# Performance work log

Measured on AMD Instinct MI355X. Metric: run time of the kernel, lower is better.

Reference implementation:

```python
import jax, jax.numpy as jnp
import numpy as np
from bisect import bisect

# hyperparameters (from init_kwargs)
DELTA = 1e-4
GAMMA = 0.1
UTILITY_SCALE = -0.01
PRIORITY_RAIL = 0.5
LOSS_BALANCE = 1.0
ALPHA_ELU = 1.0
ENTROPY_THRESHOLDS = [0, 10, 50]
ENTROPY_LEVELS = [0.0, 0.05, 0.1, 1.0]
MASK_LEVEL = 10000.0

N = 512


def setup_inputs() -> dict:
    key = jax.random.key(0)
    k1, k2, k3, k4 = jax.random.split(key, 4)
    soft_adj = jax.random.uniform(k1, (N, N), dtype=jnp.float32)
    # original adjacency is a binary {0,1} float mask
    original_adj = (jax.random.uniform(k2, (N, N)) > 0.5).astype(jnp.float32)
    distances = jax.random.uniform(k3, (N, N), dtype=jnp.float32) * 100.0
    flow = jax.random.uniform(k4, (N, N), dtype=jnp.float32) * 10.0
    epoch = 20  # python int, selects entropy penalty level via bisect
    return {"soft_adj": soft_adj, "original_adj": original_adj,
            "distances": distances, "flow": flow, "epoch": epoch}


def _shortest_path(soft_adj, distances):
    """Soft (softmin via logsumexp) Floyd-Warshall all-pairs shortest path."""
    W = distances / (soft_adj + DELTA)          # [N, N] effective edge weights
    n = W.shape[0]
    w0 = W * (1.0 - jnp.eye(n, dtype=W.dtype))  # zero diagonal

    def step(w, k):
        # softmin(w, w[:,k,None] + w[None,k,:]) without materializing a stack
        path_through_k = w[:, k][:, None] + w[k, :][None, :]
        w_new = -GAMMA * jnp.logaddexp(-w / GAMMA, -path_through_k / GAMMA)
        return w_new, None

    w_dist, _ = jax.lax.scan(step, w0, jnp.arange(n))
    return w_dist


def reference(soft_adj, original_adj, distances, flow, epoch):
    loss_cost = jnp.sum(soft_adj * distances)

    shortest_paths = _shortest_path(soft_adj, distances)

    exp_ut_rail = jnp.exp(UTILITY_SCALE * shortest_paths * PRIORITY_RAIL)
    exp_ut_base = jnp.exp(UTILITY_SCALE * distances)
    choice_matrix = exp_ut_rail / (exp_ut_rail + exp_ut_base)
    distance_saved = distances - PRIORITY_RAIL * shortest_paths
    utility_gain = flow * choice_matrix * distance_saved
    utility_gain = jax.nn.elu(utility_gain, alpha=ALPHA_ELU) + ALPHA_ELU

    inverse_soft = jnp.eye(soft_adj.shape[0], dtype=soft_adj.dtype) - soft_adj
    entropy_loss = jnp.sum(jnp.square(soft_adj * inverse_soft))
    entropy_scale = ENTROPY_LEVELS[bisect(ENTROPY_THRESHOLDS, epoch)]

    mask_loss = jnp.sum(soft_adj * (1.0 - original_adj))

    return (loss_cost
            + LOSS_BALANCE * jnp.sum(utility_gain)
            + entropy_loss * entropy_scale
            + MASK_LEVEL * mask_loss)
```

## Files before the change

kernel.cpp:

```cpp
#include <hip/hip_runtime.h>
#include <math.h>

#define NN 512
#define KP 64
#define NPANEL 8
#define NTHR 256
#define NBLK 256
#define TRUNITS (448 * 112)

#define D_   0
#define V_   4160
#define B2_  8320
#define UB_  12672
#define SB_  17024
#define H_   21376
#define LDSN 25728

__device__ __forceinline__ float einit(const float* s, const float* dI, int i, int j) {
  float w = dI[i * NN + j] / (s[i * NN + j] + 1e-4f);
  if (i == j) w = 0.f;
  return expf(-10.f * w);
}

template <int M0, int M1>
__device__ __forceinline__ void evolve_seg(float* lds, float (&x)[64], int tid) {
#pragma unroll
  for (int m = M0; m < M1; ++m) {
    const float xm = x[m];
    lds[H_ + m * 68 + tid] = xm;
#pragma unroll
    for (int a = m + 1; a < 64; ++a) {
      const int sa = __builtin_amdgcn_readlane(__float_as_int(x[a]), m);
      x[a] += __int_as_float(sa) * xm;
    }
  }
}

__device__ __forceinline__ void pgemm_chunk(float* lds, int cch, int tt2, int h) {
  const int mb = cch * 16;
  const int r = 32 * h + (tt2 & 31);
  const int g = tt2 >> 5;
  const int m0c = mb + 4 * g;
  const int vb = V_ + r * 65;
  float a0 = lds[vb + m0c + 0], a1 = lds[vb + m0c + 1];
  float a2 = lds[vb + m0c + 2], a3 = lds[vb + m0c + 3];
  for (int mp = 0; mp < mb; ++mp) {
    const float vr = lds[vb + mp];
    const float4 u4 = *(const float4*)&lds[H_ + mp * 68 + m0c];
    a0 += vr * u4.x; a1 += vr * u4.y; a2 += vr * u4.z; a3 += vr * u4.w;
  }
  lds[vb + m0c + 0] = a0; lds[vb + m0c + 1] = a1;
  lds[vb + m0c + 2] = a2; lds[vb + m0c + 3] = a3;
}

__device__ __forceinline__ void micro_chunk(float* lds, int cch, int t3, int h) {
  const int mb = cch * 16;
  const int r = 32 * h + t3;
  const int vb = V_ + r * 65 + mb;
  float v[16];
#pragma unroll
  for (int u2 = 0; u2 < 16; ++u2) v[u2] = lds[vb + u2];
#pragma unroll
  for (int mp = 0; mp < 15; ++mp) {
    const float vmp = v[mp];
#pragma unroll
    for (int m2 = mp + 1; m2 < 16; ++m2)
      v[m2] += vmp * lds[H_ + (mb + mp) * 68 + (mb + m2)];
  }
#pragma unroll
  for (int u2 = 0; u2 < 16; ++u2) lds[vb + u2] = v[u2];
}

__global__ __launch_bounds__(NTHR) void fw_phase(
    const float* __restrict__ s, const float* __restrict__ dI,
    float* __restrict__ E, float* __restrict__ Cs, float* __restrict__ Rs,
    float* __restrict__ out, int p) {
  __shared__ __align__(16) float lds[LDSN];
  const int blk = blockIdx.x, tid = threadIdx.x;
  const int k0 = p * KP;

  if (blk >= 32) {
    const int gt = (blk - 32) * NTHR + tid;
    if (p == 0) {
      if (blk == 32 && tid == 0) out[0] = 0.f;
      if (gt < TRUNITS) {
        const int ii = gt / 112;
        const int jj = gt - ii * 112;
        const int i = ii + KP;
        const int j = (jj + 16) << 2;
        const int idx = i * NN + j;
        const float4 sv = *(const float4*)(s + idx);
        const float4 dv = *(const float4*)(dI + idx);
        float w0 = dv.x / (sv.x + 1e-4f); if (i == j + 0) w0 = 0.f;
        float w1 = dv.y / (sv.y + 1e-4f); if (i == j + 1) w1 = 0.f;
        float w2 = dv.z / (sv.z + 1e-4f); if (i == j + 2) w2 = 0.f;
        float w3 = dv.w / (sv.w + 1e-4f); if (i == j + 3) w3 = 0.f;
        *(float4*)(E + idx) = make_float4(expf(-10.f * w0), expf(-10.f * w1),
                                          expf(-10.f * w2), expf(-10.f * w3));
      }
    } else if (gt < TRUNITS) {
      const int ii = gt / 112;
      const int jj = gt - ii * 112;
      const int i = (ii < k0) ? ii : ii + KP;
      const int j = ((jj < (p << 4)) ? jj : jj + 16) << 2;
      const int idx = i * NN + j;
      const float* Cprev = Cs + (size_t)(p - 1) * (NN * KP);
      const float* Rprev = Rs + (size_t)(p - 1) * (KP * NN);
      float4 acc = *(const float4*)(E + idx);
      const float* crow = Cprev + (size_t)i * KP;
      const float* rcol = Rprev + j;
#pragma unroll 8
      for (int r = 0; r < KP; ++r) {
        const float cv = crow[r];
        const float4 rv = *(const float4*)(rcol + (size_t)r * NN);
        acc.x += cv * rv.x; acc.y += cv * rv.y;
        acc.z += cv * rv.z; acc.w += cv * rv.w;
      }
      *(float4*)(E + idx) = acc;
    }
    return;
  }

  const bool isC = (blk < 16);
  const int sb = (blk >> 1) & 7;
  const int h = blk & 1;
  const int sOff = sb * KP;
  const bool haveSl = (sb != p);
  const float* Cprev = Cs + (size_t)(p - 1) * (NN * KP);
  const float* Rprev = Rs + (size_t)(p - 1) * (KP * NN);

  if (p == 0) {
    for (int e = tid; e < 4096; e += NTHR) {
      const int a = e >> 6, b = e & 63;
      const float v = einit(s, dI, a, b);
      lds[D_ + a * 65 + b] = v;
      if (blk == 0) E[a * NN + b] = v;
    }
    if (haveSl) {
      if (isC) {
        for (int e = tid; e < 2048; e += NTHR) {
          const int a = 32 * h + (e >> 6), b = e & 63;
          const float v = einit(s, dI, sOff + a, b);
          lds[V_ + a * 65 + b] = v;
          E[(sOff + a) * NN + b] = v;
        }
      } else {
        for (int e = tid; e < 2048; e += NTHR) {
          const int m = e >> 5, j = 32 * h + (e & 31);
          const float v = einit(s, dI, m, sOff + j);
          lds[V_ + j * 65 + m] = v;
          E[m * NN + (sOff + j)] = v;
        }
      }
    }
  } else {
#pragma unroll
    for (int k = 0; k < 4; ++k) {
      const int e4 = tid + k * NTHR;
      const int a = e4 >> 4, b4 = (e4 & 15) << 2;
      *(float4*)&lds[B2_ + a * 68 + b4] =
          *(const float4*)(Cprev + (size_t)(k0 + a) * KP + b4);
      *(float4*)&lds[UB_ + a * 68 + b4] =
          *(const float4*)(Rprev + (size_t)a * NN + (k0 + b4));
      if (haveSl) {
        if (isC)
          *(float4*)&lds[SB_ + a * 68 + b4] =
              *(const float4*)(Cprev + (size_t)(sOff + a) * KP + b4);
        else
          *(float4*)&lds[SB_ + a * 68 + b4] =
              *(const float4*)(Rprev + (size_t)a * NN + (sOff + b4));
      }
    }
    __syncthreads();
    {
      const int r0 = (tid >> 4) << 2, m0 = (tid & 15) << 2;
      float acc[4][4];
#pragma unroll
      for (int i2 = 0; i2 < 4; ++i2) {
        const float4 ev = *(const float4*)(E + (size_t)(k0 + r0 + i2) * NN + (k0 + m0));
        acc[i2][0] = ev.x; acc[i2][1] = ev.y; acc[i2][2] = ev.z; acc[i2][3] = ev.w;
      }
      for (int rr = 0; rr < KP; rr += 4) {
        float4 av[4];
#pragma unroll
        for (int i2 = 0; i2 < 4; ++i2)
          av[i2] = *(const float4*)&lds[B2_ + (r0 + i2) * 68 + rr];
#pragma unroll
        for (int k = 0; k < 4; ++k) {
          const float4 b4 = *(const float4*)&lds[UB_ + (rr + k) * 68 + m0];
#pragma unroll
          for (int i2 = 0; i2 < 4; ++i2) {
            const float a = (k == 0) ? av[i2].x : (k == 1) ? av[i2].y
                          : (k == 2) ? av[i2].z : av[i2].w;
            acc[i2][0] += a * b4.x; acc[i2][1] += a * b4.y;
            acc[i2][2] += a * b4.z; acc[i2][3] += a * b4.w;
          }
        }
      }
#pragma unroll
      for (int i2 = 0; i2 < 4; ++i2)
#pragma unroll
        for (int j2 = 0; j2 < 4; ++j2)
          lds[D_ + (r0 + i2) * 65 + (m0 + j2)] = acc[i2][j2];
    }
  }
  __syncthreads();

  float x[64];
  if (tid < 64) {
    if (isC) {
#pragma unroll
      for (int a = 0; a < 64; ++a) x[a] = lds[D_ + a * 65 + tid];
    } else {
#pragma unroll
      for (int a = 0; a < 64; ++a) x[a] = lds[D_ + tid * 65 + a];
    }
    evolve_seg<0, 16>(lds, x, tid);
  } else if (tid < 192) {
    const int tt = tid - 64;
    if (haveSl && p > 0) {
      float acc[4][4];
      if (isC) {
        const int r0 = 32 * h + ((tt >> 4) << 2);
        const int m0 = (tt & 15) << 2;
#pragma unroll
        for (int i2 = 0; i2 < 4; ++i2) {
          const float4 ev = *(const float4*)(E + (size_t)(sOff + r0 + i2) * NN + (k0 + m0));
          acc[i2][0] = ev.x; acc[i2][1] = ev.y; acc[i2][2] = ev.z; acc[i2][3] = ev.w;
        }
        for (int rr = 0; rr < KP; rr += 4) {
          float4 av[4];
#pragma unroll
          for (int i2 = 0; i2 < 4; ++i2)
            av[i2] = *(const float4*)&lds[SB_ + (r0 + i2) * 68 + rr];
#pragma unroll
          for (int k = 0; k < 4; ++k) {
            const float4 b4 = *(const float4*)&lds[UB_ + (rr + k) * 68 + m0];
#pragma unroll
            for (int i2 = 0; i2 < 4; ++i2) {
              const float a = (k == 0) ? av[i2].x : (k == 1) ? av[i2].y
                            : (k == 2) ? av[i2].z : av[i2].w;
              acc[i2][0] += a * b4.x; acc[i2][1] += a * b4.y;
              acc[i2][2] += a * b4.z; acc[i2][3] += a * b4.w;
            }
          }
        }
#pragma unroll
        for (int i2 = 0; i2 < 4; ++i2) {
          *(float4*)(E + (size_t)(sOff + r0 + i2) * NN + (k0 + m0)) =
              make_float4(acc[i2][0], acc[i2][1], acc[i2][2], acc[i2][3]);
#pragma unroll
          for (int j2 = 0; j2 < 4; ++j2)
            lds[V_ + (r0 + i2) * 65 + (m0 + j2)] = acc[i2][j2];
        }
      } else {
        const int r0 = (tt & 15) << 2;
        const int c0 = 32 * h + ((tt >> 4) << 2);
#pragma unroll
        for (int i2 = 0; i2 < 4; ++i2) {
          const float4 ev = *(const float4*)(E + (size_t)(k0 + r0 + i2) * NN + (sOff + c0));
          acc[i2][0] = ev.x; acc[i2][1] = ev.y; acc[i2][2] = ev.z; acc[i2][3] = ev.w;
        }
        for (int rr = 0; rr < KP; rr += 4) {
          float4 av[4];
#pragma unroll
          for (int i2 = 0; i2 < 4; ++i2)
            av[i2] = *(const float4*)&lds[B2_ + (r0 + i2) * 68 + rr];
#pragma unroll
          for (int k = 0; k < 4; ++k) {
            const float4 b4 = *(const float4*)&lds[SB_ + (rr + k) * 68 + c0];
#pragma unroll
            for (int i2 = 0; i2 < 4; ++i2) {
              const float a = (k == 0) ? av[i2].x : (k == 1) ? av[i2].y
                            : (k == 2) ? av[i2].z : av[i2].w;
              acc[i2][0] += a * b4.x; acc[i2][1] += a * b4.y;
              acc[i2][2] += a * b4.z; acc[i2][3] += a * b4.w;
            }
          }
        }
#pragma unroll
        for (int i2 = 0; i2 < 4; ++i2) {
          *(float4*)(E + (size_t)(k0 + r0 + i2) * NN + (sOff + c0)) =
              make_float4(acc[i2][0], acc[i2][1], acc[i2][2], acc[i2][3]);
#pragma unroll
          for (int j2 = 0; j2 < 4; ++j2)
            lds[V_ + (c0 + j2) * 65 + (r0 + i2)] = acc[i2][j2];
        }
      }
    } else if (!haveSl) {
      for (int e = tt; e < 4096; e += 128) {
        const int a = e >> 6, b = e & 63;
        lds[V_ + a * 65 + b] = isC ? lds[D_ + a * 65 + b] : lds[D_ + b * 65 + a];
      }
    }
  }
  __syncthreads();

  if (tid < 64) evolve_seg<16, 32>(lds, x, tid);
  else if (tid >= 192 && tid < 224) micro_chunk(lds, 0, tid - 192, h);
  __syncthreads();

  if (tid < 64) evolve_seg<32, 48>(lds, x, tid);
  else if (tid < 192) pgemm_chunk(lds, 1, tid - 64, h);
  __syncthreads();

  if (tid < 64) evolve_seg<48, 64>(lds, x, tid);
  else if (tid >= 192 && tid < 224) micro_chunk(lds, 1, tid - 192, h);
  __syncthreads();

  if (tid >= 64 && tid < 192) pgemm_chunk(lds, 2, tid - 64, h);
  __syncthreads();
  if (tid >= 192 && tid < 224) micro_chunk(lds, 2, tid - 192, h);
  __syncthreads();
  if (tid >= 64 && tid < 192) pgemm_chunk(lds, 3, tid - 64, h);
  __syncthreads();
  if (tid >= 192 && tid < 224) micro_chunk(lds, 3, tid - 192, h);
  __syncthreads();

  float* Cp = Cs + (size_t)p * (NN * KP);
  float* Rp = Rs + (size_t)p * (KP * NN);
  if (isC) {
    for (int e = tid; e < 2048; e += NTHR) {
      const int a = 32 * h + (e >> 6), b = e & 63;
      Cp[(size_t)(sOff + a) * KP + b] = lds[V_ + a * 65 + b];
    }
  } else {
    for (int e = tid; e < 2048; e += NTHR) {
      const int m = e >> 5, j = 32 * h + (e & 31);
      Rp[(size_t)m * NN + (sOff + j)] = lds[V_ + j * 65 + m];
    }
  }
}

__device__ __forceinline__ float loss_elem(float Ev, float sv, float ov,
                                           float dv, float fv, int i, int j,
                                           float esc) {
  const float sp = (Ev > 0.f) ? (-0.1f * logf(Ev)) : 1e9f;
  const float ur = expf(-0.005f * sp);
  const float ub = expf(-0.01f * dv);
  const float choice = ur / (ur + ub);
  const float ug = fv * choice * (dv - 0.5f * sp);
  const float util = (ug > 0.f) ? (ug + 1.f) : expf(ug);
  const float ent = sv * (((i == j) ? 1.f : 0.f) - sv);
  return sv * dv + util + esc * ent * ent + 10000.f * (sv * (1.f - ov));
}

__global__ __launch_bounds__(NTHR) void k_loss(
    const float* __restrict__ s, const float* __restrict__ o,
    const float* __restrict__ dI, const float* __restrict__ f,
    const int* __restrict__ ep, const float* __restrict__ E,
    const float* __restrict__ Cs, const float* __restrict__ Rs,
    float* __restrict__ out) {
  __shared__ float red[NTHR];
  const int tid = threadIdx.x;
  const int g = blockIdx.x * NTHR + tid;
  const int idx0 = g * 4;
  const int i = idx0 >> 9;
  const int j = idx0 & (NN - 1);
  const float* C7 = Cs + (size_t)7 * (NN * KP);
  const float* R7 = Rs + (size_t)7 * (KP * NN);
  float4 acc = *(const float4*)(E + idx0);
  {
    const float* crow = C7 + (size_t)i * KP;
    const float* rcol = R7 + j;
#pragma unroll 8
    for (int r = 0; r < KP; ++r) {
      const float cv = crow[r];
      const float4 rv = *(const float4*)(rcol + (size_t)r * NN);
      acc.x += cv * rv.x; acc.y += cv * rv.y;
      acc.z += cv * rv.z; acc.w += cv * rv.w;
    }
  }
  const int bi = i >> 6, bj = j >> 6;
  if (bi == bj && bi >= 1) {
    const float* cf = Cs + (size_t)(bi - 1) * (NN * KP) + (size_t)i * KP;
    const float* rf = Rs + (size_t)(bi - 1) * (KP * NN) + j;
#pragma unroll 8
    for (int r = 0; r < KP; ++r) {
      const float cv = cf[r];
      const float4 rv = *(const float4*)(rf + (size_t)r * NN);
      acc.x += cv * rv.x; acc.y += cv * rv.y;
      acc.z += cv * rv.z; acc.w += cv * rv.w;
    }
  }
  const float4 sv = *(const float4*)(s + idx0);
  const float4 ov = *(const float4*)(o + idx0);
  const float4 dv = *(const float4*)(dI + idx0);
  const float4 fv = *(const float4*)(f + idx0);
  const int e = ep[0];
  const float esc = (e < 0) ? 0.f : (e < 10) ? 0.05f : (e < 50) ? 0.1f : 1.f;
  float lsum = loss_elem(acc.x, sv.x, ov.x, dv.x, fv.x, i, j + 0, esc)
             + loss_elem(acc.y, sv.y, ov.y, dv.y, fv.y, i, j + 1, esc)
             + loss_elem(acc.z, sv.z, ov.z, dv.z, fv.z, i, j + 2, esc)
             + loss_elem(acc.w, sv.w, ov.w, dv.w, fv.w, i, j + 3, esc);
  red[tid] = lsum;
  __syncthreads();
#pragma unroll
  for (int st = 128; st > 0; st >>= 1) {
    if (tid < st) red[tid] += red[tid + st];
    __syncthreads();
  }
  if (tid == 0) atomicAdd(out, red[0]);
}

extern "C" void kernel_launch(void* const* d_in, const int* in_sizes, int n_in,
                              void* d_out, int out_size, void* d_ws, size_t ws_size,
                              hipStream_t stream) {
  const float* s = (const float*)d_in[0];
  const float* o = (const float*)d_in[1];
  const float* d = (const float*)d_in[2];
  const float* f = (const float*)d_in[3];
  const int* ep = (const int*)d_in[4];

  float* E = (float*)d_ws;
  float* Cs = E + NN * NN;
  float* Rs = Cs + NPANEL * NN * KP;
  float* out = (float*)d_out;

  for (int p = 0; p < NPANEL; ++p)
    fw_phase<<<NBLK, NTHR, 0, stream>>>(s, d, E, Cs, Rs, out, p);
  k_loss<<<NBLK, NTHR, 0, stream>>>(s, o, d, f, ep, E, Cs, Rs, out);
}
```

Before: 220.4 us.

## Fuse panel phases and loss into one cooperative kernel with grid syncs

Replaces nine separate kernel launches (eight Floyd-Warshall panel phases plus the loss reduction) with a single cooperative launch that loops over panels and separates them with grid-wide syncs. The aim is to remove per-launch overhead and the drain between dependent kernels. If the cooperative launch fails, it falls back to the original multi-launch path. Grid sync has its own cost, and all 256 blocks with large LDS use must be co-resident. The loss stage reuses the panel LDS buffer for its reduction.

```diff
diff --git a/kernel.cpp b/kernel.cpp
--- a/kernel.cpp
+++ b/kernel.cpp
@@ -1,5 +1,8 @@
 #include <hip/hip_runtime.h>
+#include <hip/hip_cooperative_groups.h>
 #include <math.h>
+
+namespace cg = cooperative_groups;
 
 #define NN 512
 #define KP 64
@@ -71,56 +74,57 @@
   for (int u2 = 0; u2 < 16; ++u2) lds[vb + u2] = v[u2];
 }
 
-__global__ __launch_bounds__(NTHR) void fw_phase(
-    const float* __restrict__ s, const float* __restrict__ dI,
-    float* __restrict__ E, float* __restrict__ Cs, float* __restrict__ Rs,
-    float* __restrict__ out, int p) {
-  __shared__ __align__(16) float lds[LDSN];
-  const int blk = blockIdx.x, tid = threadIdx.x;
+__device__ __forceinline__ void trailing_body(
+    int p, int blk, int tid, const float* __restrict__ s,
+    const float* __restrict__ dI, float* __restrict__ E,
+    const float* __restrict__ Cs, const float* __restrict__ Rs,
+    float* __restrict__ out) {
+  const int gt = (blk - 32) * NTHR + tid;
   const int k0 = p * KP;
-
-  if (blk >= 32) {
-    const int gt = (blk - 32) * NTHR + tid;
-    if (p == 0) {
-      if (blk == 32 && tid == 0) out[0] = 0.f;
-      if (gt < TRUNITS) {
-        const int ii = gt / 112;
-        const int jj = gt - ii * 112;
-        const int i = ii + KP;
-        const int j = (jj + 16) << 2;
-        const int idx = i * NN + j;
-        const float4 sv = *(const float4*)(s + idx);
-        const float4 dv = *(const float4*)(dI + idx);
-        float w0 = dv.x / (sv.x + 1e-4f); if (i == j + 0) w0 = 0.f;
-        float w1 = dv.y / (sv.y + 1e-4f); if (i == j + 1) w1 = 0.f;
-        float w2 = dv.z / (sv.z + 1e-4f); if (i == j + 2) w2 = 0.f;
-        float w3 = dv.w / (sv.w + 1e-4f); if (i == j + 3) w3 = 0.f;
-        *(float4*)(E + idx) = make_float4(expf(-10.f * w0), expf(-10.f * w1),
-                                          expf(-10.f * w2), expf(-10.f * w3));
-      }
-    } else if (gt < TRUNITS) {
+  if (p == 0) {
+    if (blk == 32 && tid == 0) out[0] = 0.f;
+    if (gt < TRUNITS) {
       const int ii = gt / 112;
       const int jj = gt - ii * 112;
-      const int i = (ii < k0) ? ii : ii + KP;
-      const int j = ((jj < (p << 4)) ? jj : jj + 16) << 2;
+      const int i = ii + KP;
+      const int j = (jj + 16) << 2;
       const int idx = i * NN + j;
-      const float* Cprev = Cs + (size_t)(p - 1) * (NN * KP);
-      const float* Rprev = Rs + (size_t)(p - 1) * (KP * NN);
-      float4 acc = *(const float4*)(E + idx);
-      const float* crow = Cprev + (size_t)i * KP;
-      const float* rcol = Rprev + j;
+      const float4 sv = *(const float4*)(s + idx);
+      const float4 dv = *(const float4*)(dI + idx);
+      float w0 = dv.x / (sv.x + 1e-4f); if (i == j + 0) w0 = 0.f;
+      float w1 = dv.y / (sv.y + 1e-4f); if (i == j + 1) w1 = 0.f;
+      float w2 = dv.z / (sv.z + 1e-4f); if (i == j + 2) w2 = 0.f;
+      float w3 = dv.w / (sv.w + 1e-4f); if (i == j + 3) w3 = 0.f;
+      *(float4*)(E + idx) = make_float4(expf(-10.f * w0), expf(-10.f * w1),
+                                        expf(-10.f * w2), expf(-10.f * w3));
+    }
+  } else if (gt < TRUNITS) {
+    const int ii = gt / 112;
+    const int jj = gt - ii * 112;
+    const int i = (ii < k0) ? ii : ii + KP;
+    const int j = ((jj < (p << 4)) ? jj : jj + 16) << 2;
+    const int idx = i * NN + j;
+    const float* Cprev = Cs + (size_t)(p - 1) * (NN * KP);
+    const float* Rprev = Rs + (size_t)(p - 1) * (KP * NN);
+    float4 acc = *(const float4*)(E + idx);
+    const float* crow = Cprev + (size_t)i * KP;
+    const float* rcol = Rprev + j;
 #pragma unroll 8
-      for (int r = 0; r < KP; ++r) {
-        const float cv = crow[r];
-        const float4 rv = *(const float4*)(rcol + (size_t)r * NN);
-        acc.x += cv * rv.x; acc.y += cv * rv.y;
-        acc.z += cv * rv.z; acc.w += cv * rv.w;
-      }
-      *(float4*)(E + idx) = acc;
-    }
-    return;
-  }
-
+    for (int r = 0; r < KP; ++r) {
+      const float cv = crow[r];
+      const float4 rv = *(const float4*)(rcol + (size_t)r * NN);
+      acc.x += cv * rv.x; acc.y += cv * rv.y;
+      acc.z += cv * rv.z; acc.w += cv * rv.w;
+    }
+    *(float4*)(E + idx) = acc;
+  }
+}
+
+__device__ __forceinline__ void panel_body(
+    int p, int blk, int tid, const float* __restrict__ s,
+    const float* __restrict__ dI, float* __restrict__ E,
+    float* __restrict__ Cs, float* __restrict__ Rs, float* lds) {
+  const int k0 = p * KP;
   const bool isC = (blk < 16);
   const int sb = (blk >> 1) & 7;
   const int h = blk & 1;
@@ -345,15 +349,13 @@
   return sv * dv + util + esc * ent * ent + 10000.f * (sv * (1.f - ov));
 }
 
-__global__ __launch_bounds__(NTHR) void k_loss(
-    const float* __restrict__ s, const float* __restrict__ o,
+__device__ __forceinline__ void loss_body(
+    int blk, int tid, const float* __restrict__ s, const float* __restrict__ o,
     const float* __restrict__ dI, const float* __restrict__ f,
     const int* __restrict__ ep, const float* __restrict__ E,
     const float* __restrict__ Cs, const float* __restrict__ Rs,
-    float* __restrict__ out) {
-  __shared__ float red[NTHR];
-  const int tid = threadIdx.x;
-  const int g = blockIdx.x * NTHR + tid;
+    float* __restrict__ out, float* red) {
+  const int g = blk * NTHR + tid;
   const int idx0 = g * 4;
   const int i = idx0 >> 9;
   const int j = idx0 & (NN - 1);
@@ -403,6 +405,43 @@
   if (tid == 0) atomicAdd(out, red[0]);
 }
 
+__global__ __launch_bounds__(NTHR) void fw_fused(
+    const float* __restrict__ s, const float* __restrict__ o,
+    const float* __restrict__ dI, const float* __restrict__ f,
+    const int* __restrict__ ep, float* __restrict__ E,
+    float* __restrict__ Cs, float* __restrict__ Rs,
+    float* __restrict__ out) {
+  cg::grid_group grid = cg::this_grid();
+  __shared__ __align__(16) float lds[LDSN];
+  const int blk = blockIdx.x, tid = threadIdx.x;
+  for (int p = 0; p < NPANEL; ++p) {
+    if (blk >= 32) trailing_body(p, blk, tid, s, dI, E, Cs, Rs, out);
+    else           panel_body(p, blk, tid, s, dI, E, Cs, Rs, lds);
+    grid.sync();
+  }
+  loss_body(blk, tid, s, o, dI, f, ep, E, Cs, Rs, out, lds);
+}
+
+__global__ __launch_bounds__(NTHR) void fw_phase(
+    const float* __restrict__ s, const float* __restrict__ dI,
+    float* __restrict__ E, float* __restrict__ Cs, float* __restrict__ Rs,
+    float* __restrict__ out, int p) {
+  __shared__ __align__(16) float lds[LDSN];
+  const int blk = blockIdx.x, tid = threadIdx.x;
+  if (blk >= 32) trailing_body(p, blk, tid, s, dI, E, Cs, Rs, out);
+  else           panel_body(p, blk, tid, s, dI, E, Cs, Rs, lds);
+}
+
+__global__ __launch_bounds__(NTHR) void k_loss(
+    const float* __restrict__ s, const float* __restrict__ o,
+    const float* __restrict__ dI, const float* __restrict__ f,
+    const int* __restrict__ ep, const float* __restrict__ E,
+    const float* __restrict__ Cs, const float* __restrict__ Rs,
+    float* __restrict__ out) {
+  __shared__ float red[NTHR];
+  loss_body(blockIdx.x, threadIdx.x, s, o, dI, f, ep, E, Cs, Rs, out, red);
+}
+
 extern "C" void kernel_launch(void* const* d_in, const int* in_sizes, int n_in,
                               void* d_out, int out_size, void* d_ws, size_t ws_size,
                               hipStream_t stream) {
@@ -417,7 +456,14 @@
   float* Rs = Cs + NPANEL * NN * KP;
   float* out = (float*)d_out;
 
-  for (int p = 0; p < NPANEL; ++p)
-    fw_phase<<<NBLK, NTHR, 0, stream>>>(s, d, E, Cs, Rs, out, p);
-  k_loss<<<NBLK, NTHR, 0, stream>>>(s, o, d, f, ep, E, Cs, Rs, out);
-}
+  void* args[] = {(void*)&s, (void*)&o, (void*)&d, (void*)&f, (void*)&ep,
+                  (void*)&E, (void*)&Cs, (void*)&Rs, (void*)&out};
+  hipError_t err = hipLaunchCooperativeKernel((const void*)fw_fused,
+                                              dim3(NBLK), dim3(NTHR),
+                                              args, 0, stream);
+  if (err != hipSuccess) {
+    for (int p = 0; p < NPANEL; ++p)
+      fw_phase<<<NBLK, NTHR, 0, stream>>>(s, d, E, Cs, Rs, out, p);
+    k_loss<<<NBLK, NTHR, 0, stream>>>(s, o, d, f, ep, E, Cs, Rs, out);
+  }
+}
```

Result: slower. 485.2 us (+120.2%).

## Split panel evolve across two waves and use wavefront readlane substitution

Applied to the files above, without the earlier changes.

Rewrites the in-panel triangular evolve so the 64-column elimination is split into upper and lower halves handled by different wavefronts. The lower wave applies the upper block's update via readlane. The separate pgemm and micro-chunk forward substitution steps are replaced by a readlane-based substitution across lanes in waves 1-2. This cuts the sequence of barriers from eight to three and balances work across waves. In exchange it does redundant multiply-by-zero work for masked lanes and uses more registers.

```diff
diff --git a/kernel.cpp b/kernel.cpp
--- a/kernel.cpp
+++ b/kernel.cpp
@@ -22,53 +22,58 @@
   return expf(-10.f * w);
 }
 
-template <int M0, int M1>
-__device__ __forceinline__ void evolve_seg(float* lds, float (&x)[64], int tid) {
-#pragma unroll
-  for (int m = M0; m < M1; ++m) {
+__device__ __forceinline__ void evolve_upper(float* lds, float (&x)[32], int lane) {
+#pragma unroll
+  for (int m = 0; m < 32; ++m) {
     const float xm = x[m];
-    lds[H_ + m * 68 + tid] = xm;
-#pragma unroll
-    for (int a = m + 1; a < 64; ++a) {
+    lds[H_ + m * 68 + lane] = xm;
+#pragma unroll
+    for (int a = m + 1; a < 32; ++a) {
       const int sa = __builtin_amdgcn_readlane(__float_as_int(x[a]), m);
       x[a] += __int_as_float(sa) * xm;
     }
   }
 }
 
-__device__ __forceinline__ void pgemm_chunk(float* lds, int cch, int tt2, int h) {
-  const int mb = cch * 16;
-  const int r = 32 * h + (tt2 & 31);
-  const int g = tt2 >> 5;
-  const int m0c = mb + 4 * g;
-  const int vb = V_ + r * 65;
-  float a0 = lds[vb + m0c + 0], a1 = lds[vb + m0c + 1];
-  float a2 = lds[vb + m0c + 2], a3 = lds[vb + m0c + 3];
-  for (int mp = 0; mp < mb; ++mp) {
-    const float vr = lds[vb + mp];
-    const float4 u4 = *(const float4*)&lds[H_ + mp * 68 + m0c];
-    a0 += vr * u4.x; a1 += vr * u4.y; a2 += vr * u4.z; a3 += vr * u4.w;
-  }
-  lds[vb + m0c + 0] = a0; lds[vb + m0c + 1] = a1;
-  lds[vb + m0c + 2] = a2; lds[vb + m0c + 3] = a3;
-}
-
-__device__ __forceinline__ void micro_chunk(float* lds, int cch, int t3, int h) {
-  const int mb = cch * 16;
-  const int r = 32 * h + t3;
-  const int vb = V_ + r * 65 + mb;
-  float v[16];
-#pragma unroll
-  for (int u2 = 0; u2 < 16; ++u2) v[u2] = lds[vb + u2];
-#pragma unroll
-  for (int mp = 0; mp < 15; ++mp) {
-    const float vmp = v[mp];
-#pragma unroll
-    for (int m2 = mp + 1; m2 < 16; ++m2)
-      v[m2] += vmp * lds[H_ + (mb + mp) * 68 + (mb + m2)];
-  }
-#pragma unroll
-  for (int u2 = 0; u2 < 16; ++u2) lds[vb + u2] = v[u2];
+__device__ __forceinline__ void evolve_lower(float* lds, float (&x)[32], int lane) {
+  float hreg[32];
+#pragma unroll
+  for (int m = 0; m < 32; ++m) hreg[m] = lds[H_ + m * 68 + lane];
+#pragma unroll
+  for (int m = 0; m < 32; ++m) {
+    const float hm = hreg[m];
+#pragma unroll
+    for (int a = 0; a < 32; ++a) {
+      const int sa = __builtin_amdgcn_readlane(__float_as_int(x[a]), m);
+      x[a] += __int_as_float(sa) * hm;
+    }
+  }
+#pragma unroll
+  for (int m = 32; m < 64; ++m) {
+    const float xm = x[m - 32];
+    lds[H_ + m * 68 + lane] = xm;
+#pragma unroll
+    for (int a = m - 32 + 1; a < 32; ++a) {
+      const int sa = __builtin_amdgcn_readlane(__float_as_int(x[a]), m);
+      x[a] += __int_as_float(sa) * xm;
+    }
+  }
+}
+
+template <int M0, int M1>
+__device__ __forceinline__ void subst_seg(float* lds, float (&x)[16], int lane) {
+  float hreg[M1 - M0];
+#pragma unroll
+  for (int m = M0; m < M1; ++m) hreg[m - M0] = lds[H_ + m * 68 + lane];
+#pragma unroll
+  for (int m = M0; m < M1; ++m) {
+    const float hm = (lane > m) ? hreg[m - M0] : 0.f;
+#pragma unroll
+    for (int r = 0; r < 16; ++r) {
+      const int sa = __builtin_amdgcn_readlane(__float_as_int(x[r]), m);
+      x[r] += __int_as_float(sa) * hm;
+    }
+  }
 }
 
 __global__ __launch_bounds__(NTHR) void fw_phase(
@@ -206,17 +211,31 @@
   }
   __syncthreads();
 
-  float x[64];
-  if (tid < 64) {
+  const int lane = tid & 63;
+  const int wv = tid >> 6;
+  float xu[32];
+  float xl[32];
+  float vs[16];
+  const int r0v = 32 * h + 16 * (wv - 1);
+
+  if (wv == 0) {
     if (isC) {
 #pragma unroll
-      for (int a = 0; a < 64; ++a) x[a] = lds[D_ + a * 65 + tid];
+      for (int a = 0; a < 32; ++a) xu[a] = lds[D_ + a * 65 + lane];
     } else {
 #pragma unroll
-      for (int a = 0; a < 64; ++a) x[a] = lds[D_ + tid * 65 + a];
-    }
-    evolve_seg<0, 16>(lds, x, tid);
-  } else if (tid < 192) {
+      for (int a = 0; a < 32; ++a) xu[a] = lds[D_ + lane * 65 + a];
+    }
+    evolve_upper(lds, xu, lane);
+  } else if (wv == 3) {
+    if (isC) {
+#pragma unroll
+      for (int a = 0; a < 32; ++a) xl[a] = lds[D_ + (32 + a) * 65 + lane];
+    } else {
+#pragma unroll
+      for (int a = 0; a < 32; ++a) xl[a] = lds[D_ + lane * 65 + (32 + a)];
+    }
+  } else {
     const int tt = tid - 64;
     if (haveSl && p > 0) {
       float acc[4][4];
@@ -296,25 +315,20 @@
   }
   __syncthreads();
 
-  if (tid < 64) evolve_seg<16, 32>(lds, x, tid);
-  else if (tid >= 192 && tid < 224) micro_chunk(lds, 0, tid - 192, h);
+  if (wv == 3) {
+    evolve_lower(lds, xl, lane);
+  } else if (wv == 1 || wv == 2) {
+#pragma unroll
+    for (int r = 0; r < 16; ++r) vs[r] = lds[V_ + (r0v + r) * 65 + lane];
+    subst_seg<0, 32>(lds, vs, lane);
+  }
   __syncthreads();
 
-  if (tid < 64) evolve_seg<32, 48>(lds, x, tid);
-  else if (tid < 192) pgemm_chunk(lds, 1, tid - 64, h);
-  __syncthreads();
-
-  if (tid < 64) evolve_seg<48, 64>(lds, x, tid);
-  else if (tid >= 192 && tid < 224) micro_chunk(lds, 1, tid - 192, h);
-  __syncthreads();
-
-  if (tid >= 64 && tid < 192) pgemm_chunk(lds, 2, tid - 64, h);
-  __syncthreads();
-  if (tid >= 192 && tid < 224) micro_chunk(lds, 2, tid - 192, h);
-  __syncthreads();
-  if (tid >= 64 && tid < 192) pgemm_chunk(lds, 3, tid - 64, h);
-  __syncthreads();
-  if (tid >= 192 && tid < 224) micro_chunk(lds, 3, tid - 192, h);
+  if (wv == 1 || wv == 2) {
+    subst_seg<32, 64>(lds, vs, lane);
+#pragma unroll
+    for (int r = 0; r < 16; ++r) lds[V_ + (r0v + r) * 65 + lane] = vs[r];
+  }
   __syncthreads();
 
   float* Cp = Cs + (size_t)p * (NN * KP);
```

Measured after the change: 276.4 us. 1.25x slower.
